# Kernel tuning notes

Measured on AMD Instinct MI355X. Metric: run time of the kernel, lower is better.

The kernel has to match this reference:

```python
import jax, jax.numpy as jnp
import numpy as np

D_MODEL = 4096
N_EXPERTS = 64
TOP_K = 2


def setup_inputs() -> dict:
    key = jax.random.key(0)
    kx, kw = jax.random.split(key)
    x = jax.random.normal(kx, (4, 8192, D_MODEL), dtype=jnp.float32)
    # nn.Linear(d_model, n_experts, bias=False) weight: [n_experts, d_model]
    W = jax.random.normal(kw, (N_EXPERTS, D_MODEL), dtype=jnp.float32) * (1.0 / np.sqrt(D_MODEL))
    return {"x": x, "W": W}


def reference(x, W):
    # logits: [B, S, n_experts]
    logits = jnp.einsum("bsd,ed->bse", x, W)
    # top-k values and indices along expert dim
    weights, experts = jax.lax.top_k(logits, TOP_K)
    weights = jax.nn.softmax(weights, axis=-1)
    return weights, experts
```

## Files before the change

kernel.cpp:

```cpp
#include <hip/hip_runtime.h>
#include <math.h>

#define D_MODEL 4096
#define N_EXP   64

typedef _Float16 half8 __attribute__((ext_vector_type(8)));
typedef float    f32x4 __attribute__((ext_vector_type(4)));

__global__ __launch_bounds__(256)
void wprep_kernel(const float* __restrict__ W,
                  _Float16* __restrict__ whf, _Float16* __restrict__ wlf) {
    const int gid   = blockIdx.x * 256 + threadIdx.x;
    const int lane  = gid & 63;
    const int ntk   = gid >> 6;
    const int nt    = ntk & 3;
    const int kstep = ntk >> 2;
    const int e  = nt * 16 + (lane & 15);
    const int k0 = kstep * 32 + (lane >> 4) * 8;

    const float* src = W + (size_t)e * D_MODEL + k0;
    float4 w0 = *(const float4*)(src);
    float4 w1 = *(const float4*)(src + 4);
    float wv[8] = {w0.x, w0.y, w0.z, w0.w, w1.x, w1.y, w1.z, w1.w};

    half8 hh, ll;
    #pragma unroll
    for (int j = 0; j < 8; ++j) {
        float ws = wv[j] * 64.0f;
        _Float16 h = (_Float16)ws;
        hh[j] = h;
        ll[j] = (_Float16)((ws - (float)h) * 4096.0f);
    }
    *(half8*)(whf + (size_t)gid * 8) = hh;
    *(half8*)(wlf + (size_t)gid * 8) = ll;
}

#define GLD16(gp, lp) __builtin_amdgcn_global_load_lds( \
    (const __attribute__((address_space(1))) unsigned int*)(const void*)(gp), \
    (__attribute__((address_space(3))) unsigned int*)(void*)(lp), 16, 0, 0)

__device__ __forceinline__ void cvt_hilo(const float4 a, const float4 b,
                                         half8& hi, half8& lo) {
    float av[8] = {a.x, a.y, a.z, a.w, b.x, b.y, b.z, b.w};
    #pragma unroll
    for (int j = 0; j < 8; ++j) {
        _Float16 h = (_Float16)av[j];
        hi[j] = h;
        lo[j] = (_Float16)((av[j] - (float)h) * 4096.0f);
    }
}

__global__ __launch_bounds__(256, 2)
void router_kernel(const float* __restrict__ x,
                   const _Float16* __restrict__ whf,
                   const _Float16* __restrict__ wlf,
                   float* __restrict__ out, int ntok) {
    __shared__ __align__(16) float     sA[2 * 4 * 4 * 260];
    __shared__ __align__(16) _Float16  sB[2][2][2][4][512];

    const int tid  = threadIdx.x;
    const int w    = tid >> 6;
    const int l    = tid & 63;
    const int tok0 = blockIdx.x * 64;

    const float* asrc0 = x + (size_t)(tok0 + w * 16 + 0 + (l >> 4)) * D_MODEL + (l & 15) * 4;
    const float* asrc1 = asrc0 + (size_t)4 * D_MODEL;
    const float* asrc2 = asrc0 + (size_t)8 * D_MODEL;
    const float* asrc3 = asrc0 + (size_t)12 * D_MODEL;
    const _Float16* bsrc = (w >> 1) ? wlf : whf;

    f32x4 hh[4], cc[4];
    #pragma unroll
    for (int nt = 0; nt < 4; ++nt) { hh[nt] = (f32x4)0.0f; cc[nt] = (f32x4)0.0f; }

#define STAGE(G, B)                                                            \
    {                                                                          \
        const int kf = (G) * 64;                  \
        GLD16(asrc0 + kf, &sA[(((B) * 4 + w) * 4 + 0) * 260]);                 \
        GLD16(asrc1 + kf, &sA[(((B) * 4 + w) * 4 + 1) * 260]);                 \
        GLD16(asrc2 + kf, &sA[(((B) * 4 + w) * 4 + 2) * 260]);                 \
        GLD16(asrc3 + kf, &sA[(((B) * 4 + w) * 4 + 3) * 260]);                 \
        const int kst = (G) * 2 + (w & 1);                                     \
        const size_t bo = (size_t)(kst * 4) * 512 + (size_t)l * 8;             \
        _Pragma("unroll")                                                      \
        for (int nt = 0; nt < 4; ++nt)                                         \
            GLD16(bsrc + bo + nt * 512, &sB[B][w & 1][w >> 1][nt][0]);         \
    }

#define STEP(KSL, CUR)                                                         \
    {                                                                          \
        const float* ap = &sA[(((CUR) * 4 + w) * 4 + ((l & 15) >> 2)) * 260    \
                              + ((l & 15) & 3) * 64 + (KSL) * 32 + (l >> 4) * 8]; \
        float4 a0 = *(const float4*)ap;                                        \
        float4 a1 = *(const float4*)(ap + 4);                                  \
        half8 ah, al;                                                          \
        cvt_hilo(a0, a1, ah, al);                                              \
        half8 bh[4], bl[4];                                                    \
        _Pragma("unroll")                                                      \
        for (int nt = 0; nt < 4; ++nt) {                                       \
            bh[nt] = *(const half8*)&sB[CUR][KSL][0][nt][l * 8];               \
            bl[nt] = *(const half8*)&sB[CUR][KSL][1][nt][l * 8];               \
        }                                                                      \
        _Pragma("unroll")                                                      \
        for (int nt = 0; nt < 4; ++nt)                                         \
            hh[nt] = __builtin_amdgcn_mfma_f32_16x16x32_f16(ah, bh[nt], hh[nt], 0, 0, 0); \
        _Pragma("unroll")                                                      \
        for (int nt = 0; nt < 4; ++nt)                                         \
            cc[nt] = __builtin_amdgcn_mfma_f32_16x16x32_f16(ah, bl[nt], cc[nt], 0, 0, 0); \
        _Pragma("unroll")                                                      \
        for (int nt = 0; nt < 4; ++nt)                                         \
            cc[nt] = __builtin_amdgcn_mfma_f32_16x16x32_f16(al, bh[nt], cc[nt], 0, 0, 0); \
    }

    STAGE(0, 0)
    __syncthreads();

    for (int gg = 0; gg < 32; ++gg) {
        const int g0 = gg * 2;
        STAGE(g0 + 1, 1)
        STEP(0, 0)
        STEP(1, 0)
        __syncthreads();
        if (g0 + 2 < 64) STAGE(g0 + 2, 0)
        STEP(0, 1)
        STEP(1, 1)
        __syncthreads();
    }
#undef STAGE
#undef STEP

    float tt[4][4];
    #pragma unroll
    for (int nt = 0; nt < 4; ++nt) {
        f32x4 tot = (hh[nt] + cc[nt] * (1.0f / 4096.0f)) * (1.0f / 64.0f);
        tt[nt][0] = tot.x; tt[nt][1] = tot.y; tt[nt][2] = tot.z; tt[nt][3] = tot.w;
    }

    float* out_e = out + (size_t)2 * ntok;

    #pragma unroll
    for (int q = 0; q < 4; ++q) {
        float v1 = -3.0e38f, v2 = -3.0e38f;
        int   i1 = 1 << 30,  i2 = 1 << 30;
        #pragma unroll
        for (int nt = 0; nt < 4; ++nt) {
            float v  = tt[nt][q];
            int   id = nt * 16 + (l & 15);
            if (v > v1 || (v == v1 && id < i1)) {
                v2 = v1; i2 = i1; v1 = v; i1 = id;
            } else if (v > v2 || (v == v2 && id < i2)) {
                v2 = v; i2 = id;
            }
        }
        #pragma unroll
        for (int m = 1; m < 16; m <<= 1) {
            float ov1 = __shfl_xor(v1, m, 64);
            int   oi1 = __shfl_xor(i1, m, 64);
            float ov2 = __shfl_xor(v2, m, 64);
            int   oi2 = __shfl_xor(i2, m, 64);
            bool ofirst = (ov1 > v1) || (ov1 == v1 && oi1 < i1);
            if (ofirst) {
                bool s2 = (ov2 > v1) || (ov2 == v1 && oi2 < i1);
                v2 = s2 ? ov2 : v1;  i2 = s2 ? oi2 : i1;
                v1 = ov1;            i1 = oi1;
            } else {
                bool s2 = (ov1 > v2) || (ov1 == v2 && oi1 < i2);
                v2 = s2 ? ov1 : v2;  i2 = s2 ? oi1 : i2;
            }
        }

        if ((l & 15) == 0) {
            const int tok = tok0 + w * 16 + (l >> 4) * 4 + q;
            float e = expf(v2 - v1);
            float d = 1.0f + e;
            out[2 * tok + 0] = 1.0f / d;
            out[2 * tok + 1] = e / d;
            out_e[2 * tok + 0] = (float)i1;
            out_e[2 * tok + 1] = (float)i2;
        }
    }
}

extern "C" void kernel_launch(void* const* d_in, const int* in_sizes, int n_in,
                              void* d_out, int out_size, void* d_ws, size_t ws_size,
                              hipStream_t stream) {
    const float* x = (const float*)d_in[0];
    const float* W = (const float*)d_in[1];
    float* out = (float*)d_out;
    const int ntok = in_sizes[0] / D_MODEL;

    _Float16* whf = (_Float16*)d_ws;
    _Float16* wlf = (_Float16*)d_ws + (size_t)N_EXP * D_MODEL;

    wprep_kernel<<<dim3(128), dim3(256), 0, stream>>>(W, whf, wlf);
    router_kernel<<<dim3(ntok / 64), dim3(256), 0, stream>>>(x, whf, wlf, out, ntok);
}
```

Measured before the change: 152.6 us.

## Use 512-thread blocks with triple-buffered LDS and partial vmcnt waits

Doubles the block to 8 waves covering 128 tokens, so the W tile staged in LDS is shared by twice as many tokens, and each wave loads only half the B fragments. The two-stage double buffer becomes a three-stage ring buffer. Each full __syncthreads is replaced by a manual s_waitcnt vmcnt(6) plus s_barrier, so one stage of global->LDS loads stays in flight while the current stage is computed. In exchange, LDS use rises to roughly 120KB per block and occupancy drops to one block per CU, and the hand-counted vmcnt must match the exact number of outstanding loads.

```diff
diff --git a/kernel.cpp b/kernel.cpp
--- a/kernel.cpp
+++ b/kernel.cpp
@@ -3,6 +3,7 @@
 
 #define D_MODEL 4096
 #define N_EXP   64
+#define SLABF   260
 
 typedef _Float16 half8 __attribute__((ext_vector_type(8)));
 typedef float    f32x4 __attribute__((ext_vector_type(4)));
@@ -50,56 +51,57 @@
     }
 }
 
-__global__ __launch_bounds__(256, 2)
+__global__ __launch_bounds__(512, 1)
 void router_kernel(const float* __restrict__ x,
                    const _Float16* __restrict__ whf,
                    const _Float16* __restrict__ wlf,
                    float* __restrict__ out, int ntok) {
-    __shared__ __align__(16) float     sA[2 * 4 * 4 * 260];
-    __shared__ __align__(16) _Float16  sB[2][2][2][4][512];
+    __shared__ __align__(16) float    sA[3 * 8 * 4 * SLABF];
+    __shared__ __align__(16) _Float16 sB[3][2][2][4][512];
 
     const int tid  = threadIdx.x;
     const int w    = tid >> 6;
     const int l    = tid & 63;
-    const int tok0 = blockIdx.x * 64;
-
-    const float* asrc0 = x + (size_t)(tok0 + w * 16 + 0 + (l >> 4)) * D_MODEL + (l & 15) * 4;
-    const float* asrc1 = asrc0 + (size_t)4 * D_MODEL;
-    const float* asrc2 = asrc0 + (size_t)8 * D_MODEL;
-    const float* asrc3 = asrc0 + (size_t)12 * D_MODEL;
-    const _Float16* bsrc = (w >> 1) ? wlf : whf;
+    const int tok0 = blockIdx.x * 128;
+
+    const float* a_s0 = x + (size_t)(tok0 + w * 16 + 0 + (l >> 4)) * D_MODEL + (l & 15) * 4;
+    const float* a_s1 = a_s0 + (size_t)4 * D_MODEL;
+    const float* a_s2 = a_s0 + (size_t)8 * D_MODEL;
+    const float* a_s3 = a_s0 + (size_t)12 * D_MODEL;
+    const int bksl = w & 1;
+    const int bhl  = (w >> 1) & 1;
+    const int bnt  = (w >> 2) * 2;
+    const _Float16* bsrc = (bhl ? wlf : whf) + (size_t)l * 8;
 
     f32x4 hh[4], cc[4];
     #pragma unroll
     for (int nt = 0; nt < 4; ++nt) { hh[nt] = (f32x4)0.0f; cc[nt] = (f32x4)0.0f; }
 
-#define STAGE(G, B)                                                            \
+#define STAGE(T, SBUF)                                                         \
     {                                                                          \
-        const int kf = (G) * 64;                  \
-        GLD16(asrc0 + kf, &sA[(((B) * 4 + w) * 4 + 0) * 260]);                 \
-        GLD16(asrc1 + kf, &sA[(((B) * 4 + w) * 4 + 1) * 260]);                 \
-        GLD16(asrc2 + kf, &sA[(((B) * 4 + w) * 4 + 2) * 260]);                 \
-        GLD16(asrc3 + kf, &sA[(((B) * 4 + w) * 4 + 3) * 260]);                 \
-        const int kst = (G) * 2 + (w & 1);                                     \
-        const size_t bo = (size_t)(kst * 4) * 512 + (size_t)l * 8;             \
-        _Pragma("unroll")                                                      \
-        for (int nt = 0; nt < 4; ++nt)                                         \
-            GLD16(bsrc + bo + nt * 512, &sB[B][w & 1][w >> 1][nt][0]);         \
-    }
-
-#define STEP(KSL, CUR)                                                         \
+        const int kf = (T) * 64;                                               \
+        GLD16(a_s0 + kf, &sA[(((SBUF) * 8 + w) * 4 + 0) * SLABF]);             \
+        GLD16(a_s1 + kf, &sA[(((SBUF) * 8 + w) * 4 + 1) * SLABF]);             \
+        GLD16(a_s2 + kf, &sA[(((SBUF) * 8 + w) * 4 + 2) * SLABF]);             \
+        GLD16(a_s3 + kf, &sA[(((SBUF) * 8 + w) * 4 + 3) * SLABF]);             \
+        const size_t bo = (size_t)(((T) * 2 + bksl) * 4 + bnt) * 512;          \
+        GLD16(bsrc + bo,       &sB[SBUF][bksl][bhl][bnt][0]);                  \
+        GLD16(bsrc + bo + 512, &sB[SBUF][bksl][bhl][bnt + 1][0]);              \
+    }
+
+#define STEP(KSL, RB)                                                          \
     {                                                                          \
-        const float* ap = &sA[(((CUR) * 4 + w) * 4 + ((l & 15) >> 2)) * 260    \
+        const float* ap = &sA[(((RB) * 8 + w) * 4 + ((l & 15) >> 2)) * SLABF   \
                               + ((l & 15) & 3) * 64 + (KSL) * 32 + (l >> 4) * 8]; \
         float4 a0 = *(const float4*)ap;                                        \
         float4 a1 = *(const float4*)(ap + 4);                                  \
-        half8 ah, al;                                                          \
-        cvt_hilo(a0, a1, ah, al);                                              \
+        half8 ah, al_;                                                         \
+        cvt_hilo(a0, a1, ah, al_);                                             \
         half8 bh[4], bl[4];                                                    \
         _Pragma("unroll")                                                      \
         for (int nt = 0; nt < 4; ++nt) {                                       \
-            bh[nt] = *(const half8*)&sB[CUR][KSL][0][nt][l * 8];               \
-            bl[nt] = *(const half8*)&sB[CUR][KSL][1][nt][l * 8];               \
+            bh[nt] = *(const half8*)&sB[RB][KSL][0][nt][l * 8];                \
+            bl[nt] = *(const half8*)&sB[RB][KSL][1][nt][l * 8];                \
         }                                                                      \
         _Pragma("unroll")                                                      \
         for (int nt = 0; nt < 4; ++nt)                                         \
@@ -109,25 +111,37 @@
             cc[nt] = __builtin_amdgcn_mfma_f32_16x16x32_f16(ah, bl[nt], cc[nt], 0, 0, 0); \
         _Pragma("unroll")                                                      \
         for (int nt = 0; nt < 4; ++nt)                                         \
-            cc[nt] = __builtin_amdgcn_mfma_f32_16x16x32_f16(al, bh[nt], cc[nt], 0, 0, 0); \
-    }
+            cc[nt] = __builtin_amdgcn_mfma_f32_16x16x32_f16(al_, bh[nt], cc[nt], 0, 0, 0); \
+    }
+
+#define SYNC6 { asm volatile("s_waitcnt vmcnt(6) lgkmcnt(0)" ::: "memory");    \
+                __builtin_amdgcn_sched_barrier(0);                             \
+                __builtin_amdgcn_s_barrier();                                  \
+                __builtin_amdgcn_sched_barrier(0); }
+#define SYNC0 { asm volatile("s_waitcnt vmcnt(0) lgkmcnt(0)" ::: "memory");    \
+                __builtin_amdgcn_sched_barrier(0);                             \
+                __builtin_amdgcn_s_barrier();                                  \
+                __builtin_amdgcn_sched_barrier(0); }
 
     STAGE(0, 0)
-    __syncthreads();
-
-    for (int gg = 0; gg < 32; ++gg) {
-        const int g0 = gg * 2;
-        STAGE(g0 + 1, 1)
-        STEP(0, 0)
-        STEP(1, 0)
-        __syncthreads();
-        if (g0 + 2 < 64) STAGE(g0 + 2, 0)
-        STEP(0, 1)
-        STEP(1, 1)
-        __syncthreads();
-    }
+    STAGE(1, 1)
+    SYNC6
+
+    for (int i = 0; i < 20; ++i) {
+        const int g = i * 3;
+        STAGE(g + 2, 2) STEP(0, 0) STEP(1, 0) SYNC6
+        STAGE(g + 3, 0) STEP(0, 1) STEP(1, 1) SYNC6
+        STAGE(g + 4, 1) STEP(0, 2) STEP(1, 2) SYNC6
+    }
+    STAGE(62, 2) STEP(0, 0) STEP(1, 0) SYNC6
+    STAGE(63, 0) STEP(0, 1) STEP(1, 1) SYNC6
+    STEP(0, 2) STEP(1, 2) SYNC0
+    STEP(0, 0) STEP(1, 0)
+
 #undef STAGE
 #undef STEP
+#undef SYNC6
+#undef SYNC0
 
     float tt[4][4];
     #pragma unroll
@@ -193,5 +207,5 @@
     _Float16* wlf = (_Float16*)d_ws + (size_t)N_EXP * D_MODEL;
 
     wprep_kernel<<<dim3(128), dim3(256), 0, stream>>>(W, whf, wlf);
-    router_kernel<<<dim3(ntok / 64), dim3(256), 0, stream>>>(x, whf, wlf, out, ntok);
-}
+    router_kernel<<<dim3(ntok / 128), dim3(512), 0, stream>>>(x, whf, wlf, out, ntok);
+}
```

Result: slower. 179.1 us (+17.4%).

## Load W directly to registers and use per-wave LDS pipeline with vmcnt waits

Applied to the files above, without the earlier changes.

Drops the shared-memory staging of the split fp16 weights. Each wave now loads its B fragments straight from global (L2) into a three-deep register rotation. The x tile moves to a per-wave, triple-buffered, XOR-swizzled LDS layout that is tracked with explicit s_waitcnt vmcnt counts and sched_barriers instead of block-wide __syncthreads. The goal is to remove block barriers and LDS bank conflicts and to overlap loads with MFMA more finely. The cost is many more VGPRs for the B buffers and a hand-counted wait schedule that is fragile to get right.

```diff
diff --git a/kernel.cpp b/kernel.cpp
--- a/kernel.cpp
+++ b/kernel.cpp
@@ -50,84 +50,114 @@
     }
 }
 
+#define MFMA16(A, B, C) __builtin_amdgcn_mfma_f32_16x16x32_f16(A, B, C, 0, 0, 0)
+
 __global__ __launch_bounds__(256, 2)
 void router_kernel(const float* __restrict__ x,
                    const _Float16* __restrict__ whf,
                    const _Float16* __restrict__ wlf,
                    float* __restrict__ out, int ntok) {
-    __shared__ __align__(16) float     sA[2 * 4 * 4 * 260];
-    __shared__ __align__(16) _Float16  sB[2][2][2][4][512];
+    __shared__ __align__(16) float sA[4][3][1024];
 
     const int tid  = threadIdx.x;
     const int w    = tid >> 6;
     const int l    = tid & 63;
     const int tok0 = blockIdx.x * 64;
-
-    const float* asrc0 = x + (size_t)(tok0 + w * 16 + 0 + (l >> 4)) * D_MODEL + (l & 15) * 4;
-    const float* asrc1 = asrc0 + (size_t)4 * D_MODEL;
-    const float* asrc2 = asrc0 + (size_t)8 * D_MODEL;
-    const float* asrc3 = asrc0 + (size_t)12 * D_MODEL;
-    const _Float16* bsrc = (w >> 1) ? wlf : whf;
+    const int hi   = l >> 4;
+    const int r    = l & 15;
+
+    const float* asrc[4];
+    #pragma unroll
+    for (int j = 0; j < 4; ++j) {
+        const int row = tok0 + w * 16 + j * 4 + hi;
+        const int csl = (l & 15) ^ (hi * 2 + (j & 1));
+        asrc[j] = x + (size_t)row * D_MODEL + csl * 4;
+    }
+
+    const int jp = r >> 2, up = r & 3;
+    const int fp = up * 2 + (jp & 1);
+    const int c1 = (hi * 2) ^ fp;
+    const float* rda = &sA[w][0][jp * 256 + up * 64 + c1 * 4];
+    const float* rdb = &sA[w][0][jp * 256 + up * 64 + (c1 ^ 1) * 4];
+
+    const _Float16* bh = whf + (size_t)l * 8;
+    const _Float16* bl = wlf + (size_t)l * 8;
 
     f32x4 hh[4], cc[4];
     #pragma unroll
     for (int nt = 0; nt < 4; ++nt) { hh[nt] = (f32x4)0.0f; cc[nt] = (f32x4)0.0f; }
 
-#define STAGE(G, B)                                                            \
-    {                                                                          \
-        const int kf = (G) * 64;                  \
-        GLD16(asrc0 + kf, &sA[(((B) * 4 + w) * 4 + 0) * 260]);                 \
-        GLD16(asrc1 + kf, &sA[(((B) * 4 + w) * 4 + 1) * 260]);                 \
-        GLD16(asrc2 + kf, &sA[(((B) * 4 + w) * 4 + 2) * 260]);                 \
-        GLD16(asrc3 + kf, &sA[(((B) * 4 + w) * 4 + 3) * 260]);                 \
-        const int kst = (G) * 2 + (w & 1);                                     \
-        const size_t bo = (size_t)(kst * 4) * 512 + (size_t)l * 8;             \
-        _Pragma("unroll")                                                      \
-        for (int nt = 0; nt < 4; ++nt)                                         \
-            GLD16(bsrc + bo + nt * 512, &sB[B][w & 1][w >> 1][nt][0]);         \
-    }
-
-#define STEP(KSL, CUR)                                                         \
-    {                                                                          \
-        const float* ap = &sA[(((CUR) * 4 + w) * 4 + ((l & 15) >> 2)) * 260    \
-                              + ((l & 15) & 3) * 64 + (KSL) * 32 + (l >> 4) * 8]; \
-        float4 a0 = *(const float4*)ap;                                        \
-        float4 a1 = *(const float4*)(ap + 4);                                  \
-        half8 ah, al;                                                          \
-        cvt_hilo(a0, a1, ah, al);                                              \
-        half8 bh[4], bl[4];                                                    \
+    half8 B0h[4], B0l[4], B1h[4], B1l[4], B2h[4], B2l[4];
+
+#define LOADB(KS, BH, BL)                                                      \
+    {                                                                          \
+        const size_t o = (size_t)(KS) * 2048;                                  \
         _Pragma("unroll")                                                      \
         for (int nt = 0; nt < 4; ++nt) {                                       \
-            bh[nt] = *(const half8*)&sB[CUR][KSL][0][nt][l * 8];               \
-            bl[nt] = *(const half8*)&sB[CUR][KSL][1][nt][l * 8];               \
+            BH[nt] = *(const half8*)(bh + o + nt * 512);                       \
+            BL[nt] = *(const half8*)(bl + o + nt * 512);                       \
         }                                                                      \
-        _Pragma("unroll")                                                      \
-        for (int nt = 0; nt < 4; ++nt)                                         \
-            hh[nt] = __builtin_amdgcn_mfma_f32_16x16x32_f16(ah, bh[nt], hh[nt], 0, 0, 0); \
-        _Pragma("unroll")                                                      \
-        for (int nt = 0; nt < 4; ++nt)                                         \
-            cc[nt] = __builtin_amdgcn_mfma_f32_16x16x32_f16(ah, bl[nt], cc[nt], 0, 0, 0); \
-        _Pragma("unroll")                                                      \
-        for (int nt = 0; nt < 4; ++nt)                                         \
-            cc[nt] = __builtin_amdgcn_mfma_f32_16x16x32_f16(al, bh[nt], cc[nt], 0, 0, 0); \
-    }
-
-    STAGE(0, 0)
-    __syncthreads();
-
-    for (int gg = 0; gg < 32; ++gg) {
-        const int g0 = gg * 2;
-        STAGE(g0 + 1, 1)
-        STEP(0, 0)
-        STEP(1, 0)
-        __syncthreads();
-        if (g0 + 2 < 64) STAGE(g0 + 2, 0)
-        STEP(0, 1)
-        STEP(1, 1)
-        __syncthreads();
-    }
-#undef STAGE
-#undef STEP
+        __builtin_amdgcn_sched_barrier(0);                                     \
+    }
+
+#define STAGEA(G, SLOT)                                                        \
+    {                                                                          \
+        const size_t go = (size_t)(G) * 64;                                    \
+        GLD16(asrc[0] + go, &sA[w][SLOT][0 * 256]);                            \
+        GLD16(asrc[1] + go, &sA[w][SLOT][1 * 256]);                            \
+        GLD16(asrc[2] + go, &sA[w][SLOT][2 * 256]);                            \
+        GLD16(asrc[3] + go, &sA[w][SLOT][3 * 256]);                            \
+        __builtin_amdgcn_sched_barrier(0);                                     \
+    }
+
+#define WAITV(N)                                                               \
+    {                                                                          \
+        asm volatile("s_waitcnt vmcnt(" #N ")" ::: "memory");                  \
+        __builtin_amdgcn_sched_barrier(0);                                     \
+    }
+
+#define KSTEP(SLOT, P, BH, BL)                                                 \
+    {                                                                          \
+        float4 a0 = *(const float4*)(rda + (SLOT) * 1024 + (P) * 32);          \
+        float4 a1 = *(const float4*)(rdb + (SLOT) * 1024 + (P) * 32);          \
+        half8 ah, al_;                                                         \
+        cvt_hilo(a0, a1, ah, al_);                                             \
+        _Pragma("unroll")                                                      \
+        for (int nt = 0; nt < 4; ++nt) hh[nt] = MFMA16(ah, BH[nt], hh[nt]);    \
+        _Pragma("unroll")                                                      \
+        for (int nt = 0; nt < 4; ++nt) cc[nt] = MFMA16(ah, BL[nt], cc[nt]);    \
+        _Pragma("unroll")                                                      \
+        for (int nt = 0; nt < 4; ++nt) cc[nt] = MFMA16(al_, BH[nt], cc[nt]);   \
+        __builtin_amdgcn_sched_barrier(0);                                     \
+    }
+
+    STAGEA(0, 0) STAGEA(1, 1)
+    LOADB(0, B0h, B0l) LOADB(1, B1h, B1l) LOADB(2, B2h, B2l)
+
+    WAITV(16) STAGEA(2, 2) KSTEP(0, 0, B0h, B0l) LOADB(3, B0h, B0l)
+
+    for (int m = 0; m < 20; ++m) {
+        const int t = 6 * m;
+        WAITV(20)                    KSTEP(0, 1, B1h, B1l) LOADB(t + 4, B1h, B1l)
+        WAITV(20) STAGEA(3 * m + 3, 0) KSTEP(1, 0, B2h, B2l) LOADB(t + 5, B2h, B2l)
+        WAITV(20)                    KSTEP(1, 1, B0h, B0l) LOADB(t + 6, B0h, B0l)
+        WAITV(20) STAGEA(3 * m + 4, 1) KSTEP(2, 0, B1h, B1l) LOADB(t + 7, B1h, B1l)
+        WAITV(20)                    KSTEP(2, 1, B2h, B2l) LOADB(t + 8, B2h, B2l)
+        WAITV(20) STAGEA(3 * m + 5, 2) KSTEP(0, 0, B0h, B0l) LOADB(t + 9, B0h, B0l)
+    }
+
+    WAITV(20)               KSTEP(0, 1, B1h, B1l) LOADB(124, B1h, B1l)
+    WAITV(20) STAGEA(63, 0) KSTEP(1, 0, B2h, B2l) LOADB(125, B2h, B2l)
+    WAITV(20)               KSTEP(1, 1, B0h, B0l) LOADB(126, B0h, B0l)
+    WAITV(20)               KSTEP(2, 0, B1h, B1l) LOADB(127, B1h, B1l)
+    WAITV(16)               KSTEP(2, 1, B2h, B2l)
+    WAITV(8)                KSTEP(0, 0, B0h, B0l)
+    WAITV(0)                KSTEP(0, 1, B1h, B1l)
+
+#undef LOADB
+#undef STAGEA
+#undef WAITV
+#undef KSTEP
 
     float tt[4][4];
     #pragma unroll
```

Result: slower. 174.1 us (+14.1%).

## Split K across two wave groups and stream x directly into registers

Applied to the files above, without the earlier changes.

The router kernel now uses 512 threads, with two wave groups each covering half of the 4096-wide reduction dimension. The x tile no longer goes through LDS. Each lane loads its MFMA operand straight from global memory into registers, prefetched four k-steps ahead. W tiles are still double-buffered in LDS, synchronised with explicit vmcnt waits and barriers, and the two K-halves are combined through LDS before top-2 selection. The aim is to raise memory-level parallelism and occupancy for this bandwidth-bound GEMV-like pass, at the cost of more registers and an extra reduction step.

```diff
diff --git a/kernel.cpp b/kernel.cpp
--- a/kernel.cpp
+++ b/kernel.cpp
@@ -50,89 +50,123 @@
     }
 }
 
-__global__ __launch_bounds__(256, 2)
+#define MFMA16(A, B, C) __builtin_amdgcn_mfma_f32_16x16x32_f16(A, B, C, 0, 0, 0)
+
+__global__ __launch_bounds__(512, 4)
 void router_kernel(const float* __restrict__ x,
                    const _Float16* __restrict__ whf,
                    const _Float16* __restrict__ wlf,
                    float* __restrict__ out, int ntok) {
-    __shared__ __align__(16) float     sA[2 * 4 * 4 * 260];
-    __shared__ __align__(16) _Float16  sB[2][2][2][4][512];
+    __shared__ __align__(16) _Float16 sB[2][2][2][2][4][512];
 
     const int tid  = threadIdx.x;
     const int w    = tid >> 6;
     const int l    = tid & 63;
+    const int st   = w & 3;
+    const int kh   = w >> 2;
     const int tok0 = blockIdx.x * 64;
 
-    const float* asrc0 = x + (size_t)(tok0 + w * 16 + 0 + (l >> 4)) * D_MODEL + (l & 15) * 4;
-    const float* asrc1 = asrc0 + (size_t)4 * D_MODEL;
-    const float* asrc2 = asrc0 + (size_t)8 * D_MODEL;
-    const float* asrc3 = asrc0 + (size_t)12 * D_MODEL;
-    const _Float16* bsrc = (w >> 1) ? wlf : whf;
+    const float* ax = x + (size_t)(tok0 + st * 16 + (l & 15)) * D_MODEL
+                        + kh * 2048 + (l >> 4) * 8;
+
+    const int ksl = st & 1;
+    const int hl  = st >> 1;
+    const _Float16* bsrc = (hl ? wlf : whf) + (size_t)(kh * 64) * 2048 + (size_t)l * 8;
 
     f32x4 hh[4], cc[4];
     #pragma unroll
     for (int nt = 0; nt < 4; ++nt) { hh[nt] = (f32x4)0.0f; cc[nt] = (f32x4)0.0f; }
 
-#define STAGE(G, B)                                                            \
-    {                                                                          \
-        const int kf = (G) * 64;                  \
-        GLD16(asrc0 + kf, &sA[(((B) * 4 + w) * 4 + 0) * 260]);                 \
-        GLD16(asrc1 + kf, &sA[(((B) * 4 + w) * 4 + 1) * 260]);                 \
-        GLD16(asrc2 + kf, &sA[(((B) * 4 + w) * 4 + 2) * 260]);                 \
-        GLD16(asrc3 + kf, &sA[(((B) * 4 + w) * 4 + 3) * 260]);                 \
-        const int kst = (G) * 2 + (w & 1);                                     \
-        const size_t bo = (size_t)(kst * 4) * 512 + (size_t)l * 8;             \
-        _Pragma("unroll")                                                      \
-        for (int nt = 0; nt < 4; ++nt)                                         \
-            GLD16(bsrc + bo + nt * 512, &sB[B][w & 1][w >> 1][nt][0]);         \
-    }
-
-#define STEP(KSL, CUR)                                                         \
-    {                                                                          \
-        const float* ap = &sA[(((CUR) * 4 + w) * 4 + ((l & 15) >> 2)) * 260    \
-                              + ((l & 15) & 3) * 64 + (KSL) * 32 + (l >> 4) * 8]; \
-        float4 a0 = *(const float4*)ap;                                        \
-        float4 a1 = *(const float4*)(ap + 4);                                  \
-        half8 ah, al;                                                          \
-        cvt_hilo(a0, a1, ah, al);                                              \
-        half8 bh[4], bl[4];                                                    \
+    float4 R0a, R0b, R1a, R1b, R2a, R2b, R3a, R3b;
+
+#define STAGE(G, BUF)                                                          \
+    {                                                                          \
+        const size_t so = (size_t)(2 * (G) + ksl) * 2048;                      \
+        GLD16(bsrc + so + 0 * 512, &sB[kh][BUF][ksl][hl][0][0]);               \
+        GLD16(bsrc + so + 1 * 512, &sB[kh][BUF][ksl][hl][1][0]);               \
+        GLD16(bsrc + so + 2 * 512, &sB[kh][BUF][ksl][hl][2][0]);               \
+        GLD16(bsrc + so + 3 * 512, &sB[kh][BUF][ksl][hl][3][0]);               \
+    }
+
+#define REFILL(T, RA, RB)                                                      \
+    {                                                                          \
+        RA = *(const float4*)(ax + (size_t)(T) * 32);                          \
+        RB = *(const float4*)(ax + (size_t)(T) * 32 + 4);                      \
+    }
+
+#define KSTEP(RA, RB, KSL_, BUF)                                               \
+    {                                                                          \
+        half8 ah, al_;                                                         \
+        cvt_hilo(RA, RB, ah, al_);                                             \
         _Pragma("unroll")                                                      \
         for (int nt = 0; nt < 4; ++nt) {                                       \
-            bh[nt] = *(const half8*)&sB[CUR][KSL][0][nt][l * 8];               \
-            bl[nt] = *(const half8*)&sB[CUR][KSL][1][nt][l * 8];               \
+            half8 bh = *(const half8*)&sB[kh][BUF][KSL_][0][nt][l * 8];        \
+            half8 bl = *(const half8*)&sB[kh][BUF][KSL_][1][nt][l * 8];        \
+            hh[nt] = MFMA16(ah, bh, hh[nt]);                                   \
+            cc[nt] = MFMA16(ah, bl, cc[nt]);                                   \
+            cc[nt] = MFMA16(al_, bh, cc[nt]);                                  \
         }                                                                      \
-        _Pragma("unroll")                                                      \
-        for (int nt = 0; nt < 4; ++nt)                                         \
-            hh[nt] = __builtin_amdgcn_mfma_f32_16x16x32_f16(ah, bh[nt], hh[nt], 0, 0, 0); \
-        _Pragma("unroll")                                                      \
-        for (int nt = 0; nt < 4; ++nt)                                         \
-            cc[nt] = __builtin_amdgcn_mfma_f32_16x16x32_f16(ah, bl[nt], cc[nt], 0, 0, 0); \
-        _Pragma("unroll")                                                      \
-        for (int nt = 0; nt < 4; ++nt)                                         \
-            cc[nt] = __builtin_amdgcn_mfma_f32_16x16x32_f16(al, bh[nt], cc[nt], 0, 0, 0); \
+    }
+
+#define SYNCN(N)                                                               \
+    {                                                                          \
+        asm volatile("s_waitcnt vmcnt(" #N ") lgkmcnt(0)" ::: "memory");       \
+        __builtin_amdgcn_sched_barrier(0);                                     \
+        __builtin_amdgcn_s_barrier();                                          \
+        __builtin_amdgcn_sched_barrier(0);                                     \
     }
 
     STAGE(0, 0)
+    REFILL(0, R0a, R0b) REFILL(1, R1a, R1b)
+    REFILL(2, R2a, R2b) REFILL(3, R3a, R3b)
+    SYNCN(8)
+
+    for (int g = 0; g < 30; g += 2) {
+        STAGE(g + 1, 1)
+        KSTEP(R0a, R0b, 0, 0)
+        REFILL(2 * g + 4, R0a, R0b)
+        KSTEP(R1a, R1b, 1, 0)
+        REFILL(2 * g + 5, R1a, R1b)
+        SYNCN(4)
+
+        STAGE(g + 2, 0)
+        KSTEP(R2a, R2b, 0, 1)
+        REFILL(2 * g + 6, R2a, R2b)
+        KSTEP(R3a, R3b, 1, 1)
+        REFILL(2 * g + 7, R3a, R3b)
+        SYNCN(4)
+    }
+    STAGE(31, 1)
+    KSTEP(R0a, R0b, 0, 0)
+    KSTEP(R1a, R1b, 1, 0)
+    SYNCN(0)
+    KSTEP(R2a, R2b, 0, 1)
+    KSTEP(R3a, R3b, 1, 1)
+    SYNCN(0)
+
+#undef STAGE
+#undef REFILL
+#undef KSTEP
+#undef SYNCN
+
+    f32x4 pt[4];
+    #pragma unroll
+    for (int nt = 0; nt < 4; ++nt) pt[nt] = hh[nt] + cc[nt] * (1.0f / 4096.0f);
+
+    float* red = (float*)&sB[0][0][0][0][0][0];
+    if (kh == 1) {
+        #pragma unroll
+        for (int nt = 0; nt < 4; ++nt)
+            *(f32x4*)&red[(size_t)(nt * 256 + st * 64 + l) * 4] = pt[nt];
+    }
     __syncthreads();
-
-    for (int gg = 0; gg < 32; ++gg) {
-        const int g0 = gg * 2;
-        STAGE(g0 + 1, 1)
-        STEP(0, 0)
-        STEP(1, 0)
-        __syncthreads();
-        if (g0 + 2 < 64) STAGE(g0 + 2, 0)
-        STEP(0, 1)
-        STEP(1, 1)
-        __syncthreads();
-    }
-#undef STAGE
-#undef STEP
+    if (kh == 1) return;
 
     float tt[4][4];
     #pragma unroll
     for (int nt = 0; nt < 4; ++nt) {
-        f32x4 tot = (hh[nt] + cc[nt] * (1.0f / 4096.0f)) * (1.0f / 64.0f);
+        f32x4 oth = *(const f32x4*)&red[(size_t)(nt * 256 + st * 64 + l) * 4];
+        f32x4 tot = (pt[nt] + oth) * (1.0f / 64.0f);
         tt[nt][0] = tot.x; tt[nt][1] = tot.y; tt[nt][2] = tot.z; tt[nt][3] = tot.w;
     }
 
@@ -170,7 +204,7 @@
         }
 
         if ((l & 15) == 0) {
-            const int tok = tok0 + w * 16 + (l >> 4) * 4 + q;
+            const int tok = tok0 + st * 16 + (l >> 4) * 4 + q;
             float e = expf(v2 - v1);
             float d = 1.0f + e;
             out[2 * tok + 0] = 1.0f / d;
@@ -193,5 +227,5 @@
     _Float16* wlf = (_Float16*)d_ws + (size_t)N_EXP * D_MODEL;
 
     wprep_kernel<<<dim3(128), dim3(256), 0, stream>>>(W, whf, wlf);
-    router_kernel<<<dim3(ntok / 64), dim3(256), 0, stream>>>(x, whf, wlf, out, ntok);
-}
+    router_kernel<<<dim3(ntok / 64), dim3(512), 0, stream>>>(x, whf, wlf, out, ntok);
+}
```

Result: faster. 135.9 us (-10.9%).
